# Optimization experiments

Hardware: AMD Instinct MI355X
Metric: run time of the kernel (lower is better)

The kernel has to match this reference:

```python
import jax, jax.numpy as jnp
import numpy as np

THETA = 10000.0
NUM_HEADS = 16
MAX_SEQ_LEN = 2048

def _rope_tables(d_k, max_seq_len, theta=THETA):
    dims = jnp.arange(0, d_k, 2, dtype=jnp.float32)
    freqs = 1.0 / theta ** (dims / d_k)
    t = jnp.arange(max_seq_len, dtype=jnp.float32)
    angles = jnp.outer(t, freqs)  # (max_seq_len, d_k//2)
    return jnp.cos(angles), jnp.sin(angles)

def _apply_rope(x, token_positions, cos_tab, sin_tab):
    # x: (..., seq_len, d_k)
    cos = jnp.repeat(cos_tab[token_positions], 2, axis=-1)  # (seq_len, d_k)
    sin = jnp.repeat(sin_tab[token_positions], 2, axis=-1)
    # interleaved rotate-half: (-x1, x0, -x3, x2, ...)
    xp = x.reshape(*x.shape[:-1], -1, 2)
    x_neg = jnp.stack([-xp[..., 1], xp[..., 0]], axis=-1).reshape(x.shape)
    return x * cos + x_neg * sin

def setup_inputs() -> dict:
    key = jax.random.key(0)
    ks = jax.random.split(key, 5)
    B, S, D = 4, 2048, 1024
    scale = 1.0 / np.sqrt(D)
    return {
        "x": jax.random.normal(ks[0], (B, S, D), dtype=jnp.float32),
        "q_proj": jax.random.normal(ks[1], (D, D), dtype=jnp.float32) * scale,
        "k_proj": jax.random.normal(ks[2], (D, D), dtype=jnp.float32) * scale,
        "v_proj": jax.random.normal(ks[3], (D, D), dtype=jnp.float32) * scale,
        "o_proj": jax.random.normal(ks[4], (D, D), dtype=jnp.float32) * scale,
        "token_positions": jnp.arange(S, dtype=jnp.int64),
    }

def reference(x, q_proj, k_proj, v_proj, o_proj, token_positions):
    B, S, D = x.shape
    H = NUM_HEADS
    d_k = D // H
    cos_tab, sin_tab = _rope_tables(d_k, MAX_SEQ_LEN)

    q = (x @ q_proj).reshape(B, S, H, d_k).transpose(0, 2, 1, 3)  # (B,H,S,d_k)
    k = (x @ k_proj).reshape(B, S, H, d_k).transpose(0, 2, 1, 3)
    v = (x @ v_proj).reshape(B, S, H, d_k).transpose(0, 2, 1, 3)

    q = _apply_rope(q, token_positions, cos_tab, sin_tab)
    k = _apply_rope(k, token_positions, cos_tab, sin_tab)

    scores = jnp.einsum('bhqd,bhkd->bhqk', q, k) / jnp.sqrt(jnp.float32(d_k))
    causal = jnp.tril(jnp.ones((S, S), dtype=bool))
    scores = jnp.where(causal, scores, -jnp.inf)
    attn = jax.nn.softmax(scores, axis=-1)
    out = jnp.einsum('bhqk,bhkd->bhqd', attn, v)  # (B,H,S,d_k)
    out = out.transpose(0, 2, 1, 3).reshape(B, S, D)
    return out @ o_proj
```

## Files before the change

### kernel.cpp

```cpp
#include <hip/hip_runtime.h>
#include <hip/hip_bf16.h>
#include <stdint.h>


typedef __attribute__((ext_vector_type(8))) short short8;
typedef __attribute__((ext_vector_type(4))) float floatx4;
typedef __attribute__((ext_vector_type(16))) float floatx16;

#define MFMA16(a,b,c) __builtin_amdgcn_mfma_f32_16x16x32_bf16((a),(b),(c),0,0,0)
#define MFMA32(a,b,c) __builtin_amdgcn_mfma_f32_32x32x16_bf16((a),(b),(c),0,0,0)
#define BAR() __builtin_amdgcn_s_barrier()
#define LGKM0 asm volatile("s_waitcnt lgkmcnt(0)" ::: "memory")
#define VMCNT4 asm volatile("s_waitcnt vmcnt(4)" ::: "memory")
#define VMCNT6 asm volatile("s_waitcnt vmcnt(6)" ::: "memory")

__device__ __forceinline__ uint32_t fbits(float f){ uint32_t u; __builtin_memcpy(&u,&f,4); return u; }
__device__ __forceinline__ unsigned short f2bf(float f) {
    uint32_t u = fbits(f);
    return (unsigned short)((u + 0x7fffu + ((u>>16)&1u)) >> 16);
}
__device__ __forceinline__ float bf2f(unsigned short s){ uint32_t u = (uint32_t)s<<16; float f; __builtin_memcpy(&f,&u,4); return f; }
__device__ __forceinline__ uint32_t pkbf(float lo, float hi) {
#if __has_builtin(__builtin_amdgcn_cvt_pk_bf16_f32)
    auto r = __builtin_amdgcn_cvt_pk_bf16_f32(lo, hi);
    uint32_t u; __builtin_memcpy(&u, &r, sizeof(u));
    return u;
#else
    return __builtin_amdgcn_perm(fbits(hi)+0x8000u, fbits(lo)+0x8000u, 0x07060302u);
#endif
}
__device__ __forceinline__ float fexp2(float x) {
#if __has_builtin(__builtin_amdgcn_exp2f)
    return __builtin_amdgcn_exp2f(x);
#else
    return exp2f(x);
#endif
}

__device__ __forceinline__ void load_lds16(const unsigned short* g, unsigned short* l) {
    __builtin_amdgcn_global_load_lds(
        (const __attribute__((address_space(1))) void*)g,
        (__attribute__((address_space(3))) void*)l, 16, 0, 0);
}

__device__ __forceinline__ bool sniff_f32(const unsigned short* xr) {
    int lane = threadIdx.x & 63;
    int bad = 0;
#pragma unroll
    for (int i = 0; i < 16; i++) {
        float v = bf2f(xr[lane * 16 + i]);
        if (!(__builtin_fabsf(v) < 1e10f)) bad = 1;
    }
    return __ballot(bad != 0) != 0ull;
}

__global__ __launch_bounds__(256) void prep_k(
    const void* __restrict__ x,
    const void* __restrict__ wq, const void* __restrict__ wk,
    const void* __restrict__ wv, const void* __restrict__ wo,
    unsigned short* __restrict__ WT, unsigned short* __restrict__ WoT,
    float2* __restrict__ tab, unsigned short* __restrict__ xb) {
    int blk = blockIdx.x, t = threadIdx.x;
    bool f32 = sniff_f32((const unsigned short*)x);
    if (blk < 4096) {
        __shared__ unsigned short tile[32][33];
        int mat = blk >> 10, r = blk & 1023;
        const void* src = (mat == 0) ? wq : (mat == 1) ? wk : (mat == 2) ? wv : wo;
        unsigned short* dst = (mat < 3) ? (WT + (size_t)mat * 1048576) : WoT;
        int bx = (r & 31) * 32, by = (r >> 5) * 32;
        int tx = t & 31, ty = t >> 5;
#pragma unroll
        for (int j = 0; j < 32; j += 8) {
            size_t idx = (size_t)(by + ty + j) * 1024 + bx + tx;
            float v = f32 ? ((const float*)src)[idx] : bf2f(((const unsigned short*)src)[idx]);
            tile[ty + j][tx] = f2bf(v);
        }
        __syncthreads();
#pragma unroll
        for (int j = 0; j < 32; j += 8)
            dst[(size_t)(bx + ty + j) * 1024 + by + tx] = tile[tx][ty + j];
    } else if (blk < 4352) {
        int i = (blk - 4096) * 256 + t;
        int pos = i >> 5, j = i & 31;
        float freq = exp2f(-(float)(2 * j) * (1.0f / 64.0f) * 13.287712379549449f);
        float a = (float)pos * freq;
        tab[i] = make_float2(cosf(a), sinf(a));
    } else {
        size_t base = (size_t)(blk - 4352) * 2048 + (size_t)t * 8;
        if (f32) {
            const float4* s4 = (const float4*)((const float*)x + base);
            float4 a = s4[0], b = s4[1];
            uint4 o;
            o.x = pkbf(a.x, a.y); o.y = pkbf(a.z, a.w);
            o.z = pkbf(b.x, b.y); o.w = pkbf(b.z, b.w);
            *(uint4*)(xb + base) = o;
        } else {
            *(uint4*)(xb + base) = *(const uint4*)((const unsigned short*)x + base);
        }
    }
}

__global__ __launch_bounds__(512, 2) void gemm32(
    const unsigned short* __restrict__ A,
    const unsigned short* __restrict__ Bt,
    unsigned short* __restrict__ C0,
    unsigned short* __restrict__ C1,
    unsigned short* __restrict__ C2,
    const float2* __restrict__ tab) {
    const int K = 1024;
    extern __shared__ __align__(16) char smraw[];
    unsigned short* SL = (unsigned short*)smraw;

    int t = threadIdx.x;
    int lane = t & 63, w = t >> 6;
    int quad = lane >> 4, l15 = lane & 15;
    int wm = (w >> 2) * 128, wn = (w & 3) * 64;

    int flat = blockIdx.y * 12 + blockIdx.x;
    int swzid = (flat & 7) * 48 + (flat >> 3);
    int bx = swzid % 12, by = swzid / 12;
    int m0 = by * 256, n0 = bx * 256;

    floatx4 acc[8][4];
#pragma unroll
    for (int i = 0; i < 8; i++)
#pragma unroll
        for (int j = 0; j < 4; j++) acc[i][j] = (floatx4){0.f, 0.f, 0.f, 0.f};

    int srow = t >> 2;
    int sg = ((t & 3) ^ ((t >> 3) & 3)) * 8;
    const unsigned short* gA = A + (size_t)(m0 + srow) * K + sg;
    const unsigned short* gB = Bt + (size_t)(n0 + srow) * K + sg;

    int colsw = (quad ^ ((l15 >> 1) & 3)) * 8;
    int rAo = (wm + l15) * 32 + colsw;
    int rBo = 8192 + (wn + l15) * 32 + colsw;

#pragma unroll
    for (int kt = 0; kt < 2; kt++) {
        unsigned short* Sb = SL + kt * 16384 + w * 512;
        load_lds16(gA + kt * 32, Sb);
        load_lds16(gA + (size_t)128 * K + kt * 32, Sb + 4096);
        load_lds16(gB + kt * 32, Sb + 8192);
        load_lds16(gB + (size_t)128 * K + kt * 32, Sb + 12288);
    }
    VMCNT4;
    __syncthreads();

    int cur = 0, nxt = 2;
#pragma unroll 1
    for (int kt = 0; kt < 32; kt++) {
        const unsigned short* cA = SL + cur * 16384 + rAo;
        const unsigned short* cB = SL + cur * 16384 + rBo;
        unsigned short* Sb = SL + nxt * 16384 + w * 512;
        int kc = (kt < 30) ? (kt + 2) : 31;
        size_t ko = (size_t)kc * 32;
        short8 af[4], bf[4];

#pragma unroll
        for (int m = 0; m < 4; m++) af[m] = *(const short8*)(cA + m * 512);
#pragma unroll
        for (int j = 0; j < 4; j++) bf[j] = *(const short8*)(cB + j * 512);
        load_lds16(gA + ko, Sb);
        load_lds16(gA + (size_t)128 * K + ko, Sb + 4096);
        BAR(); LGKM0;
        __builtin_amdgcn_s_setprio(1);
#pragma unroll
        for (int m = 0; m < 4; m++)
#pragma unroll
            for (int j = 0; j < 4; j++) acc[m][j] = MFMA16(af[m], bf[j], acc[m][j]);
        __builtin_amdgcn_s_setprio(0);
        BAR();

#pragma unroll
        for (int m = 0; m < 4; m++) af[m] = *(const short8*)(cA + (m + 4) * 512);
        load_lds16(gB + ko, Sb + 8192);
        load_lds16(gB + (size_t)128 * K + ko, Sb + 12288);
        BAR(); LGKM0;
        __builtin_amdgcn_s_setprio(1);
#pragma unroll
        for (int m = 0; m < 4; m++)
#pragma unroll
            for (int j = 0; j < 4; j++) acc[m + 4][j] = MFMA16(af[m], bf[j], acc[m + 4][j]);
        __builtin_amdgcn_s_setprio(0);
        VMCNT4;
        BAR();

        cur = (cur == 2) ? 0 : cur + 1;
        nxt = (nxt == 2) ? 0 : nxt + 1;
    }

#pragma unroll
    for (int i = 0; i < 8; i++) {
#pragma unroll
        for (int j = 0; j < 4; j++) {
            int col = n0 + wn + j * 16 + l15;
            int row0 = m0 + wm + i * 16 + quad * 4;
            int which = col >> 10, nn = col & 1023;
            int b = row0 >> 11, s0 = row0 & 2047;
            if (which == 2) {
                int hh = nn >> 6, d = nn & 63;
                uint32_t lo = pkbf(acc[i][j][0], acc[i][j][1]);
                uint32_t hi = pkbf(acc[i][j][2], acc[i][j][3]);
                *(uint64_t*)(C2 + ((size_t)((b * 16 + hh) * 64 + d)) * 2048 + s0) =
                    (uint64_t)lo | ((uint64_t)hi << 32);
            } else {
                int d = nn & 63;
                unsigned short* dst = (which == 0) ? C0 : C1;
                float sc = (which == 0) ? 0.18033688011112042f : 1.0f;
#pragma unroll
                for (int r = 0; r < 4; r++) {
                    int s = s0 + r;
                    float v = acc[i][j][r];
                    float pv = __shfl_xor(v, 1);
                    float2 cs = tab[(s << 5) + (d >> 1)];
                    float o = (d & 1) ? (v * cs.x + pv * cs.y) : (v * cs.x - pv * cs.y);
                    dst[((size_t)(b * 2048 + s)) * 1024 + nn] = f2bf(o * sc);
                }
            }
        }
    }
}

template <int MODE>
__global__ __launch_bounds__(512, 2) void gemm8(
    const unsigned short* __restrict__ A,
    const unsigned short* __restrict__ Bt,
    void* __restrict__ C0,
    unsigned short* __restrict__ C1,
    unsigned short* __restrict__ C2,
    const float2* __restrict__ tab,
    const unsigned short* __restrict__ xsniff) {
    const int K = 1024;
    extern __shared__ __align__(16) char smraw[];
    unsigned short* Asm = (unsigned short*)smraw;
    unsigned short* Bsm = Asm + 3 * 8192;

    int t = threadIdx.x;
    int lane = t & 63, w = t >> 6;
    int quad = lane >> 4, l15 = lane & 15;
    int wm = (w >> 2) * 64, wn = (w & 3) * 64;

    int nbx = gridDim.x;
    int flat = blockIdx.y * nbx + blockIdx.x;
    int cpx = (nbx * gridDim.y) >> 3;
    int swzid = (flat & 7) * cpx + (flat >> 3);
    int bx = swzid % nbx, by = swzid / nbx;
    int m0 = by * 128, n0 = bx * 256;

    floatx4 acc[4][4];
#pragma unroll
    for (int i = 0; i < 4; i++)
#pragma unroll
        for (int j = 0; j < 4; j++) acc[i][j] = (floatx4){0.f, 0.f, 0.f, 0.f};

    int srow = t >> 3;
    int sg = ((t & 7) ^ (srow & 7)) * 8;
    const unsigned short* gA = A + (size_t)(m0 + srow) * K + sg;
    const unsigned short* gB = Bt + (size_t)(n0 + srow) * K + sg;
    unsigned short* lA = Asm + w * 512;
    unsigned short* lB = Bsm + w * 512;

    int rA[4], rB[4], ce[2];
#pragma unroll
    for (int m = 0; m < 4; m++) rA[m] = (wm + m * 16 + l15) * 64;
#pragma unroll
    for (int n = 0; n < 4; n++) rB[n] = (wn + n * 16 + l15) * 64;
#pragma unroll
    for (int ks = 0; ks < 2; ks++)
        ce[ks] = ((ks * 64 + quad * 16) ^ ((l15 & 7) << 4)) >> 1;

#pragma unroll
    for (int kt = 0; kt < 2; kt++) {
#pragma unroll
        for (int h = 0; h < 2; h++)
            load_lds16(gA + (size_t)h * 64 * K + kt * 64, lA + kt * 8192 + h * 4096);
#pragma unroll
        for (int c = 0; c < 4; c++)
            load_lds16(gB + (size_t)c * 64 * K + kt * 64, lB + kt * 16384 + c * 4096);
    }
    VMCNT6;
    __syncthreads();

    int cur = 0, nxt = 2;
#pragma unroll 1
    for (int kt = 0; kt < 16; kt++) {
        const unsigned short* cA = Asm + cur * 8192;
        const unsigned short* cB = Bsm + cur * 16384;
        unsigned short* nA = lA + nxt * 8192;
        unsigned short* nB = lB + nxt * 16384;
        size_t ko = (size_t)(kt + 2) * 64;
        short8 a0[4], a1[4], bf0, bf1;

#pragma unroll
        for (int m = 0; m < 4; m++) a0[m] = *(const short8*)(cA + rA[m] + ce[0]);
        bf0 = *(const short8*)(cB + rB[0] + ce[0]);
        bf1 = *(const short8*)(cB + rB[1] + ce[0]);
        load_lds16(gA + ko, nA);
        load_lds16(gA + (size_t)64 * K + ko, nA + 4096);
        BAR(); LGKM0;
        __builtin_amdgcn_s_setprio(1);
#pragma unroll
        for (int m = 0; m < 4; m++) {
            acc[m][0] = MFMA16(a0[m], bf0, acc[m][0]);
            acc[m][1] = MFMA16(a0[m], bf1, acc[m][1]);
        }
        __builtin_amdgcn_s_setprio(0);
        BAR();

        bf0 = *(const short8*)(cB + rB[2] + ce[0]);
        bf1 = *(const short8*)(cB + rB[3] + ce[0]);
        load_lds16(gB + ko, nB);
        load_lds16(gB + (size_t)64 * K + ko, nB + 4096);
        BAR(); LGKM0;
        __builtin_amdgcn_s_setprio(1);
#pragma unroll
        for (int m = 0; m < 4; m++) {
            acc[m][2] = MFMA16(a0[m], bf0, acc[m][2]);
            acc[m][3] = MFMA16(a0[m], bf1, acc[m][3]);
        }
        __builtin_amdgcn_s_setprio(0);
        BAR();

#pragma unroll
        for (int m = 0; m < 4; m++) a1[m] = *(const short8*)(cA + rA[m] + ce[1]);
        bf0 = *(const short8*)(cB + rB[0] + ce[1]);
        bf1 = *(const short8*)(cB + rB[1] + ce[1]);
        load_lds16(gB + (size_t)128 * K + ko, nB + 8192);
        load_lds16(gB + (size_t)192 * K + ko, nB + 12288);
        BAR(); LGKM0;
        __builtin_amdgcn_s_setprio(1);
#pragma unroll
        for (int m = 0; m < 4; m++) {
            acc[m][0] = MFMA16(a1[m], bf0, acc[m][0]);
            acc[m][1] = MFMA16(a1[m], bf1, acc[m][1]);
        }
        __builtin_amdgcn_s_setprio(0);
        BAR();

        bf0 = *(const short8*)(cB + rB[2] + ce[1]);
        bf1 = *(const short8*)(cB + rB[3] + ce[1]);
        BAR(); LGKM0;
        __builtin_amdgcn_s_setprio(1);
#pragma unroll
        for (int m = 0; m < 4; m++) {
            acc[m][2] = MFMA16(a1[m], bf0, acc[m][2]);
            acc[m][3] = MFMA16(a1[m], bf1, acc[m][3]);
        }
        __builtin_amdgcn_s_setprio(0);
        VMCNT6;
        BAR();

        cur = (cur == 2) ? 0 : cur + 1;
        nxt = (nxt == 2) ? 0 : nxt + 1;
    }

    bool out_f32 = (MODE == 0) ? sniff_f32(xsniff) : false;
#pragma unroll
    for (int i = 0; i < 4; i++) {
#pragma unroll
        for (int j = 0; j < 4; j++) {
            int col = n0 + wn + j * 16 + l15;
            int row0 = m0 + wm + i * 16 + quad * 4;
            if (MODE == 0) {
#pragma unroll
                for (int r = 0; r < 4; r++) {
                    size_t idx = (size_t)(row0 + r) * 1024 + col;
                    if (out_f32) ((float*)C0)[idx] = acc[i][j][r];
                    else ((unsigned short*)C0)[idx] = f2bf(acc[i][j][r]);
                }
            } else {
                int which = col >> 10, nn = col & 1023;
                int b = row0 >> 11, s0 = row0 & 2047;
                if (which == 2) {
                    int hh = nn >> 6, d = nn & 63;
                    uint32_t lo = pkbf(acc[i][j][0], acc[i][j][1]);
                    uint32_t hi = pkbf(acc[i][j][2], acc[i][j][3]);
                    *(uint64_t*)(C2 + ((size_t)((b * 16 + hh) * 64 + d)) * 2048 + s0) =
                        (uint64_t)lo | ((uint64_t)hi << 32);
                } else {
                    int d = nn & 63;
                    unsigned short* dst = (which == 0) ? (unsigned short*)C0 : C1;
                    float sc = (which == 0) ? 0.18033688011112042f : 1.0f;
#pragma unroll
                    for (int r = 0; r < 4; r++) {
                        int s = s0 + r;
                        float v = acc[i][j][r];
                        float pv = __shfl_xor(v, 1);
                        float2 cs = tab[(s << 5) + (d >> 1)];
                        float o = (d & 1) ? (v * cs.x + pv * cs.y) : (v * cs.x - pv * cs.y);
                        dst[((size_t)(b * 2048 + s)) * 1024 + nn] = f2bf(o * sc);
                    }
                }
            }
        }
    }
}

__global__ __launch_bounds__(512, 4) void flash_k(
    const unsigned short* __restrict__ Qb,
    const unsigned short* __restrict__ Kb,
    const unsigned short* __restrict__ Vt,
    unsigned short* __restrict__ A2) {
    __shared__ __align__(16) char sm[33792];
    unsigned short* Kl = (unsigned short*)sm;
    unsigned short* Vl = (unsigned short*)(sm + 16384);
    float4* Osw = (float4*)sm;
    float*  lsw = (float*)(sm + 32768);

    int bh = blockIdx.x;
    int y = blockIdx.y;
    int qt = (y < 8) ? (15 - y) : (y - 8);
    int b = bh >> 4, h = bh & 15;
    int t = threadIdx.x, lane = t & 63, w = t >> 6;
    int wq = w & 3, wg = w >> 2;
    int l31 = lane & 31, half = lane >> 5;
    size_t base = ((size_t)b * 2048) * 1024 + h * 64;
    int q0w = qt * 128 + wq * 32;

    short8 Qf[4];
#pragma unroll
    for (int ks = 0; ks < 4; ks++)
        Qf[ks] = *(const short8*)(Qb + base + (size_t)(q0w + l31) * 1024 + ks * 16 + half * 8);

    floatx16 O[2];
    O[0] = (floatx16)0.0f; O[1] = (floatx16)0.0f;
    float lsum = 0.f;

    int nk = 2 * (qt + 1);

    int srow = t >> 3, gs = t & 7;
    const unsigned short* kg = Kb + base + (size_t)srow * 1024 + gs * 8;
    const unsigned short* vg = Vt + ((size_t)(bh * 64 + srow)) * 2048 + gs * 8;
    int sw = srow * 64 + ((gs ^ (srow & 7)) * 8);

    short8 rk = *(const short8*)(kg);
    short8 rv = *(const short8*)(vg);

    for (int kt = 0; kt < nk; kt++) {
        int k0 = kt * 64, bf = kt & 1;
        *(short8*)&Kl[bf * 4096 + sw] = rk;
        *(short8*)&Vl[bf * 4096 + sw] = rv;
        __syncthreads();
        if (kt + 1 < nk) {
            size_t ko = (size_t)(kt + 1) * 64;
            rk = *(const short8*)(kg + ko * 1024);
            rv = *(const short8*)(vg + ko);
        }
        int k0mb = k0 + wg * 32;
        if (k0mb < q0w + 32) {
            const unsigned short* Klb = Kl + bf * 4096;
            const unsigned short* Vlb = Vl + bf * 4096;
            short8 Ka[4];
#pragma unroll
            for (int ks = 0; ks < 4; ks++)
                Ka[ks] = *(const short8*)&Klb[(wg * 32 + l31) * 64 +
                                              (((ks * 2 + half) ^ (l31 & 7)) * 8)];
            floatx16 Sc = (floatx16)0.0f;
#pragma unroll
            for (int ks = 0; ks < 4; ks++)
                Sc = MFMA32(Ka[ks], Qf[ks], Sc);

            bool domask = (k0mb + 31 > q0w);
            int thr = q0w + l31 - k0mb - half * 4;
            float p[16];
#pragma unroll
            for (int e = 0; e < 16; e++) {
                float v = fexp2(Sc[e]);
                if (domask) {
                    const int ce = (e & 3) + ((e >> 2) << 3);
                    v = (ce > thr) ? 0.f : v;
                }
                p[e] = v;
            }
            float t0 = (p[0] + p[1]) + (p[2] + p[3]);
            float t1 = (p[4] + p[5]) + (p[6] + p[7]);
            float t2 = (p[8] + p[9]) + (p[10] + p[11]);
            float t3 = (p[12] + p[13]) + (p[14] + p[15]);
            lsum += (t0 + t1) + (t2 + t3);
            uint32_t pkm[8];
#pragma unroll
            for (int jj = 0; jj < 8; jj++)
                pkm[jj] = pkbf(p[2 * jj], p[2 * jj + 1]);

            short8 Va[2][2];
#pragma unroll
            for (int db = 0; db < 2; db++)
#pragma unroll
                for (int ks2 = 0; ks2 < 2; ks2++)
                    Va[db][ks2] = *(const short8*)&Vlb[(db * 32 + l31) * 64 +
                                                       ((((wg * 2 + ks2) * 2 + half) ^ (l31 & 7)) * 8)];
#pragma unroll
            for (int ks2 = 0; ks2 < 2; ks2++) {
                uint32_t p0 = pkm[4 * ks2 + 0];
                uint32_t p1 = pkm[4 * ks2 + 1];
                uint32_t p2 = pkm[4 * ks2 + 2];
                uint32_t p3 = pkm[4 * ks2 + 3];
                uint32_t u = half ? p0 : p2;
                uint32_t v2 = half ? p1 : p3;
                uint32_t ya = (uint32_t)__shfl_xor((int)u, 32);
                uint32_t yb = (uint32_t)__shfl_xor((int)v2, 32);
                union { short8 s; uint32_t q[4]; } bb;
                bb.q[0] = half ? ya : p0;
                bb.q[1] = half ? yb : p1;
                bb.q[2] = half ? p2 : ya;
                bb.q[3] = half ? p3 : yb;
#pragma unroll
                for (int db = 0; db < 2; db++)
                    O[db] = MFMA32(Va[db][ks2], bb.s, O[db]);
            }
        }
    }

    __syncthreads();
    if (w < 4) {
#pragma unroll
        for (int db = 0; db < 2; db++)
#pragma unroll
            for (int g = 0; g < 4; g++)
                Osw[(w * 8 + db * 4 + g) * 64 + lane] =
                    make_float4(O[db][g * 4 + 0], O[db][g * 4 + 1],
                                O[db][g * 4 + 2], O[db][g * 4 + 3]);
        lsw[w * 64 + lane] = lsum;
    }
    __syncthreads();
    if (w >= 4) {
        int wp = w - 4;
#pragma unroll
        for (int db = 0; db < 2; db++)
#pragma unroll
            for (int g = 0; g < 4; g++) {
                float4 o = Osw[(wp * 8 + db * 4 + g) * 64 + lane];
                O[db][g * 4 + 0] += o.x;
                O[db][g * 4 + 1] += o.y;
                O[db][g * 4 + 2] += o.z;
                O[db][g * 4 + 3] += o.w;
            }
        lsum += lsw[wp * 64 + lane];
        float tot = lsum + __shfl_xor(lsum, 32);
        float inv = 1.0f / tot;
        int scol = q0w + l31;
        unsigned short* op = A2 + base + (size_t)scol * 1024;
#pragma unroll
        for (int db = 0; db < 2; db++) {
#pragma unroll
            for (int g = 0; g < 4; g++) {
                int d0 = db * 32 + half * 4 + g * 8;
                float v0 = O[db][g * 4 + 0] * inv;
                float v1 = O[db][g * 4 + 1] * inv;
                float v2 = O[db][g * 4 + 2] * inv;
                float v3 = O[db][g * 4 + 3] * inv;
                uint32_t lo = pkbf(v0, v1), hi = pkbf(v2, v3);
                *(uint64_t*)(op + d0) = (uint64_t)lo | ((uint64_t)hi << 32);
            }
        }
    }
}

extern "C" void kernel_launch(void* const* d_in, const int* in_sizes, int n_in,
                              void* d_out, int out_size, void* d_ws, size_t ws_size,
                              hipStream_t stream) {
    const void* x  = d_in[0];
    const void* wq = d_in[1];
    const void* wk = d_in[2];
    const void* wv = d_in[3];
    const void* wo = d_in[4];

    char* ws = (char*)d_ws;
    unsigned short* WT  = (unsigned short*)(ws);
    unsigned short* WoT = (unsigned short*)(ws + 6291456);
    float2*         tab = (float2*)(ws + 8388608);
    unsigned short* xb  = (unsigned short*)(ws + 8913920);
    unsigned short* Qb  = (unsigned short*)(ws + 8913920 + 16777216ull);
    unsigned short* Kb  = (unsigned short*)(ws + 8913920 + 2ull * 16777216);
    unsigned short* Vt  = (unsigned short*)(ws + 8913920 + 3ull * 16777216);
    unsigned short* A2  = xb;

    (void)hipFuncSetAttribute(reinterpret_cast<const void*>(gemm32),
                              hipFuncAttributeMaxDynamicSharedMemorySize, 98304);
    (void)hipFuncSetAttribute(reinterpret_cast<const void*>(gemm8<0>),
                              hipFuncAttributeMaxDynamicSharedMemorySize, 147456);

    prep_k<<<8448, 256, 0, stream>>>(x, wq, wk, wv, wo, WT, WoT, tab, xb);

    gemm32<<<dim3(12, 32), 512, 98304, stream>>>(xb, WT, Qb, Kb, Vt, tab);
    flash_k<<<dim3(64, 16), 512, 0, stream>>>(Qb, Kb, Vt, A2);
    gemm8<0><<<dim3(4, 64), 512, 147456, stream>>>(A2, WoT, d_out, nullptr, nullptr, tab,
                                                   (const unsigned short*)x);
}
```

Baseline: 263.7 us.

## Shrink QKV GEMM block tile to 128x256 with 4 waves

Restructures the fused QKV projection GEMM to use 128x256 block tiles with 256 threads (4 waves, each covering all 128 rows and 64 columns), instead of 256x256 tiles with 8 waves. The grid doubles to 768 blocks and LDS per block drops to 72KB. The load schedule and vmcnt waits are adjusted to match. The aim is better wave-level occupancy and tail balance across CUs, at the cost of less operand reuse per block and more global traffic for the weight tile.

```diff
diff --git a/kernel.cpp b/kernel.cpp
--- a/kernel.cpp
+++ b/kernel.cpp
@@ -11,7 +11,6 @@
 #define MFMA32(a,b,c) __builtin_amdgcn_mfma_f32_32x32x16_bf16((a),(b),(c),0,0,0)
 #define BAR() __builtin_amdgcn_s_barrier()
 #define LGKM0 asm volatile("s_waitcnt lgkmcnt(0)" ::: "memory")
-#define VMCNT4 asm volatile("s_waitcnt vmcnt(4)" ::: "memory")
 #define VMCNT6 asm volatile("s_waitcnt vmcnt(6)" ::: "memory")
 
 __device__ __forceinline__ uint32_t fbits(float f){ uint32_t u; __builtin_memcpy(&u,&f,4); return u; }
@@ -100,7 +99,7 @@
     }
 }
 
-__global__ __launch_bounds__(512, 2) void gemm32(
+__global__ __launch_bounds__(256, 2) void gemmq(
     const unsigned short* __restrict__ A,
     const unsigned short* __restrict__ Bt,
     unsigned short* __restrict__ C0,
@@ -114,12 +113,12 @@
     int t = threadIdx.x;
     int lane = t & 63, w = t >> 6;
     int quad = lane >> 4, l15 = lane & 15;
-    int wm = (w >> 2) * 128, wn = (w & 3) * 64;
+    int wn = w * 64;
 
     int flat = blockIdx.y * 12 + blockIdx.x;
-    int swzid = (flat & 7) * 48 + (flat >> 3);
+    int swzid = (flat & 7) * 96 + (flat >> 3);
     int bx = swzid % 12, by = swzid / 12;
-    int m0 = by * 256, n0 = bx * 256;
+    int m0 = by * 128, n0 = bx * 256;
 
     floatx4 acc[8][4];
 #pragma unroll
@@ -127,63 +126,67 @@
 #pragma unroll
         for (int j = 0; j < 4; j++) acc[i][j] = (floatx4){0.f, 0.f, 0.f, 0.f};
 
-    int srow = t >> 2;
     int sg = ((t & 3) ^ ((t >> 3) & 3)) * 8;
-    const unsigned short* gA = A + (size_t)(m0 + srow) * K + sg;
-    const unsigned short* gB = Bt + (size_t)(n0 + srow) * K + sg;
+    const unsigned short* gA = A + (size_t)(m0 + (t >> 2)) * K + sg;
+    const unsigned short* gB = Bt + (size_t)(n0 + (t >> 2)) * K + sg;
 
     int colsw = (quad ^ ((l15 >> 1) & 3)) * 8;
-    int rAo = (wm + l15) * 32 + colsw;
-    int rBo = 8192 + (wn + l15) * 32 + colsw;
 
 #pragma unroll
     for (int kt = 0; kt < 2; kt++) {
-        unsigned short* Sb = SL + kt * 16384 + w * 512;
+        unsigned short* Sb = SL + kt * 12288 + w * 512;
         load_lds16(gA + kt * 32, Sb);
-        load_lds16(gA + (size_t)128 * K + kt * 32, Sb + 4096);
-        load_lds16(gB + kt * 32, Sb + 8192);
-        load_lds16(gB + (size_t)128 * K + kt * 32, Sb + 12288);
-    }
-    VMCNT4;
+        load_lds16(gA + (size_t)64 * K + kt * 32, Sb + 2048);
+        load_lds16(gB + kt * 32, Sb + 4096);
+        load_lds16(gB + (size_t)64 * K + kt * 32, Sb + 6144);
+        load_lds16(gB + (size_t)128 * K + kt * 32, Sb + 8192);
+        load_lds16(gB + (size_t)192 * K + kt * 32, Sb + 10240);
+    }
+    VMCNT6;
     __syncthreads();
 
     int cur = 0, nxt = 2;
 #pragma unroll 1
     for (int kt = 0; kt < 32; kt++) {
-        const unsigned short* cA = SL + cur * 16384 + rAo;
-        const unsigned short* cB = SL + cur * 16384 + rBo;
-        unsigned short* Sb = SL + nxt * 16384 + w * 512;
+        const unsigned short* cA = SL + cur * 12288;
+        const unsigned short* cB = SL + cur * 12288 + 4096;
+        unsigned short* Sb = SL + nxt * 12288 + w * 512;
         int kc = (kt < 30) ? (kt + 2) : 31;
         size_t ko = (size_t)kc * 32;
         short8 af[4], bf[4];
 
 #pragma unroll
-        for (int m = 0; m < 4; m++) af[m] = *(const short8*)(cA + m * 512);
-#pragma unroll
-        for (int j = 0; j < 4; j++) bf[j] = *(const short8*)(cB + j * 512);
+        for (int m = 0; m < 4; m++)
+            af[m] = *(const short8*)(cA + (m * 16 + l15) * 32 + colsw);
+#pragma unroll
+        for (int n = 0; n < 4; n++)
+            bf[n] = *(const short8*)(cB + (wn + n * 16 + l15) * 32 + colsw);
         load_lds16(gA + ko, Sb);
-        load_lds16(gA + (size_t)128 * K + ko, Sb + 4096);
+        load_lds16(gA + (size_t)64 * K + ko, Sb + 2048);
+        load_lds16(gB + ko, Sb + 4096);
         BAR(); LGKM0;
         __builtin_amdgcn_s_setprio(1);
 #pragma unroll
         for (int m = 0; m < 4; m++)
 #pragma unroll
-            for (int j = 0; j < 4; j++) acc[m][j] = MFMA16(af[m], bf[j], acc[m][j]);
+            for (int n = 0; n < 4; n++) acc[m][n] = MFMA16(af[m], bf[n], acc[m][n]);
         __builtin_amdgcn_s_setprio(0);
         BAR();
 
 #pragma unroll
-        for (int m = 0; m < 4; m++) af[m] = *(const short8*)(cA + (m + 4) * 512);
-        load_lds16(gB + ko, Sb + 8192);
-        load_lds16(gB + (size_t)128 * K + ko, Sb + 12288);
+        for (int m = 0; m < 4; m++)
+            af[m] = *(const short8*)(cA + ((m + 4) * 16 + l15) * 32 + colsw);
+        load_lds16(gB + (size_t)64 * K + ko, Sb + 6144);
+        load_lds16(gB + (size_t)128 * K + ko, Sb + 8192);
+        load_lds16(gB + (size_t)192 * K + ko, Sb + 10240);
         BAR(); LGKM0;
         __builtin_amdgcn_s_setprio(1);
 #pragma unroll
         for (int m = 0; m < 4; m++)
 #pragma unroll
-            for (int j = 0; j < 4; j++) acc[m + 4][j] = MFMA16(af[m], bf[j], acc[m + 4][j]);
+            for (int n = 0; n < 4; n++) acc[m + 4][n] = MFMA16(af[m], bf[n], acc[m + 4][n]);
         __builtin_amdgcn_s_setprio(0);
-        VMCNT4;
+        VMCNT6;
         BAR();
 
         cur = (cur == 2) ? 0 : cur + 1;
@@ -195,7 +198,7 @@
 #pragma unroll
         for (int j = 0; j < 4; j++) {
             int col = n0 + wn + j * 16 + l15;
-            int row0 = m0 + wm + i * 16 + quad * 4;
+            int row0 = m0 + i * 16 + quad * 4;
             int which = col >> 10, nn = col & 1023;
             int b = row0 >> 11, s0 = row0 & 2047;
             if (which == 2) {
@@ -576,14 +579,14 @@
     unsigned short* Vt  = (unsigned short*)(ws + 8913920 + 3ull * 16777216);
     unsigned short* A2  = xb;
 
-    (void)hipFuncSetAttribute(reinterpret_cast<const void*>(gemm32),
-                              hipFuncAttributeMaxDynamicSharedMemorySize, 98304);
+    (void)hipFuncSetAttribute(reinterpret_cast<const void*>(gemmq),
+                              hipFuncAttributeMaxDynamicSharedMemorySize, 73728);
     (void)hipFuncSetAttribute(reinterpret_cast<const void*>(gemm8<0>),
                               hipFuncAttributeMaxDynamicSharedMemorySize, 147456);
 
     prep_k<<<8448, 256, 0, stream>>>(x, wq, wk, wv, wo, WT, WoT, tab, xb);
 
-    gemm32<<<dim3(12, 32), 512, 98304, stream>>>(xb, WT, Qb, Kb, Vt, tab);
+    gemmq<<<dim3(12, 64), 256, 73728, stream>>>(xb, WT, Qb, Kb, Vt, tab);
     flash_k<<<dim3(64, 16), 512, 0, stream>>>(Qb, Kb, Vt, A2);
     gemm8<0><<<dim3(4, 64), 512, 147456, stream>>>(A2, WoT, d_out, nullptr, nullptr, tab,
                                                    (const unsigned short*)x);
```

Result: faster. 251.7 us (-4.5%).
